# Kernel tuning notes

Hardware: AMD Instinct MI355X
Metric: run time of the kernel (lower is better)

The kernel has to match this reference:

```python
import jax, jax.numpy as jnp
import numpy as np

NUM_ROUTING_ITER = 3

def _squash(x):
    # Faithful to torch x.norm(): GLOBAL Frobenius norm over the whole tensor.
    n2 = jnp.sum(x * x)
    return x * (jnp.sqrt(n2) / (1.0 + n2))

def setup_inputs() -> dict:
    key = jax.random.key(0)
    k1, k2 = jax.random.split(key)
    x = jax.random.normal(k1, (256, 1152, 8), dtype=jnp.float32)
    weight = jax.random.normal(k2, (10, 1152, 8, 16), dtype=jnp.float32)
    return {"x": x, "weight": weight}

def reference(x, weight):
    # priors: [NC, B, IC, 1, OC] from [1,B,IC,1,L] @ [NC,1,IC,L,OC]
    priors = jnp.einsum('bil,nilo->nbio', x, weight)[:, :, :, None, :]
    b = jnp.zeros_like(priors)
    v = None
    for _ in range(NUM_ROUTING_ITER):
        # legacy F.softmax with no dim on a 5D tensor -> dim=1 (batch dim)
        c = jax.nn.softmax(b, axis=1)
        s = jnp.sum(c * priors, axis=2, keepdims=True)  # [NC,B,1,1,OC]
        v = _squash(s)
        b = b + jnp.sum(priors * v, axis=-1, keepdims=True)
    return v
```

## Files before the change

kernel.cpp:

```cpp
#include <hip/hip_runtime.h>
#include <math.h>

#define NC    10
#define BATCH 256
#define IC    1152
#define LDIM  8
#define OC    16

#define NCH   96
#define CH    (IC/NCH)
#define NBLK  (NC*NCH)
#define NTHR  256
#define NTOT  (NC*BATCH*OC)
#define NRED  160
#define KPG   (NCH/4)

typedef float f32x2 __attribute__((ext_vector_type(2)));

__device__ __forceinline__ int xcd_swizzle(int bid, int nwg) {
    int cpx = nwg >> 3;
    return (bid & 7) * cpx + (bid >> 3);
}

__global__ __launch_bounds__(256) void k0_xT(const float* __restrict__ x,
                                             float* __restrict__ xT)
{
    int u = blockIdx.x * 256 + threadIdx.x;
    int i = u >> 9, r = u & 511, b = r >> 1, h = r & 1;
    reinterpret_cast<float4*>(xT)[u] =
        reinterpret_cast<const float4*>(x)[((size_t)b * IC + i) * 2 + h];
}

__global__ __launch_bounds__(256) void kA(
    const float* __restrict__ xT, const float* __restrict__ w,
    float* __restrict__ s_part)
{
    int wg = xcd_swizzle(blockIdx.x, NBLK);
    int n  = wg / NCH, ch = wg % NCH;
    int i0 = ch * CH;
    int t  = threadIdx.x;

    f32x2 sp2[8];
#pragma unroll
    for (int j = 0; j < 8; ++j) sp2[j] = (f32x2){0.f, 0.f};

    for (int ii = 0; ii < CH; ++ii) {
        int i = i0 + ii;
        const float4* xp = reinterpret_cast<const float4*>(xT)
                         + ((size_t)i * BATCH + t) * 2;
        float4 xa = xp[0], xb = xp[1];
        float xr[8] = {xa.x, xa.y, xa.z, xa.w, xb.x, xb.y, xb.z, xb.w};
        const f32x2* wp2 = reinterpret_cast<const f32x2*>(
            w + (size_t)__builtin_amdgcn_readfirstlane((n * IC + i) * (LDIM * OC)));
#pragma unroll
        for (int l = 0; l < LDIM; ++l) {
            f32x2 xl = {xr[l], xr[l]};
#pragma unroll
            for (int j = 0; j < 8; ++j)
                sp2[j] += wp2[l * 8 + j] * xl;
        }
    }
    float4* dst = reinterpret_cast<float4*>(s_part)
                + (((size_t)ch * NC + n) * BATCH + t) * 4;
    const float inv = 1.0f / 256.0f;
    dst[0] = make_float4(sp2[0].x*inv, sp2[0].y*inv, sp2[1].x*inv, sp2[1].y*inv);
    dst[1] = make_float4(sp2[2].x*inv, sp2[2].y*inv, sp2[3].x*inv, sp2[3].y*inv);
    dst[2] = make_float4(sp2[4].x*inv, sp2[4].y*inv, sp2[5].x*inv, sp2[5].y*inv);
    dst[3] = make_float4(sp2[6].x*inv, sp2[6].y*inv, sp2[7].x*inv, sp2[7].y*inv);
}

__global__ __launch_bounds__(256) void kR(const float* __restrict__ s_part,
                                          float* __restrict__ s,
                                          float* __restrict__ n2_part)
{
    __shared__ float4 lds[4][64];
    int t = threadIdx.x, lane = t & 63, g = t >> 6;
    int idx0 = blockIdx.x * 256;
    const float* base = s_part + idx0 + lane * 4;
    float4 a0 = make_float4(0,0,0,0), a1 = a0, a2 = a0, a3 = a0;
    for (int k = 0; k < KPG; k += 4) {
        float4 v0 = *reinterpret_cast<const float4*>(base + (size_t)(g*KPG + k    ) * NTOT);
        float4 v1 = *reinterpret_cast<const float4*>(base + (size_t)(g*KPG + k + 1) * NTOT);
        float4 v2 = *reinterpret_cast<const float4*>(base + (size_t)(g*KPG + k + 2) * NTOT);
        float4 v3 = *reinterpret_cast<const float4*>(base + (size_t)(g*KPG + k + 3) * NTOT);
        a0.x += v0.x; a0.y += v0.y; a0.z += v0.z; a0.w += v0.w;
        a1.x += v1.x; a1.y += v1.y; a1.z += v1.z; a1.w += v1.w;
        a2.x += v2.x; a2.y += v2.y; a2.z += v2.z; a2.w += v2.w;
        a3.x += v3.x; a3.y += v3.y; a3.z += v3.z; a3.w += v3.w;
    }
    float4 a = make_float4((a0.x+a1.x)+(a2.x+a3.x), (a0.y+a1.y)+(a2.y+a3.y),
                           (a0.z+a1.z)+(a2.z+a3.z), (a0.w+a1.w)+(a2.w+a3.w));
    lds[g][lane] = a;
    __syncthreads();
    if (t < 64) {
        float4 s0 = lds[0][t], s1 = lds[1][t], s2 = lds[2][t], s3 = lds[3][t];
        float4 sv = make_float4((s0.x+s1.x)+(s2.x+s3.x), (s0.y+s1.y)+(s2.y+s3.y),
                                (s0.z+s1.z)+(s2.z+s3.z), (s0.w+s1.w)+(s2.w+s3.w));
        *reinterpret_cast<float4*>(s + idx0 + t * 4) = sv;
        float q = sv.x*sv.x + sv.y*sv.y + sv.z*sv.z + sv.w*sv.w;
#pragma unroll
        for (int m = 32; m >= 1; m >>= 1) q += __shfl_xor(q, m, 64);
        if (t == 0) n2_part[blockIdx.x] = q;
    }
}

template<int MODE>
__global__ __launch_bounds__(256) void kB(
    const float* __restrict__ xT, const float* __restrict__ w,
    const float* __restrict__ s1, const float* __restrict__ n2p1,
    const float* __restrict__ s2, const float* __restrict__ n2p2,
    float* __restrict__ s_part)
{
    __shared__ float e_lds[CH][NTHR];
    __shared__ float esW[CH][4];
    __shared__ float redW[8];
    int t = threadIdx.x, lane = t & 63, wid = t >> 6;
    int wg = xcd_swizzle(blockIdx.x, NBLK);
    int n  = wg / NCH, ch = wg % NCH;
    int i0 = ch * CH;

    float q1 = (t < NRED) ? n2p1[t] : 0.f;
    float q2 = (MODE == 2 && t < NRED) ? n2p2[t] : 0.f;
#pragma unroll
    for (int m = 32; m >= 1; m >>= 1) {
        q1 += __shfl_xor(q1, m, 64);
        if (MODE == 2) q2 += __shfl_xor(q2, m, 64);
    }
    if (lane == 0) { redW[wid] = q1; redW[4 + wid] = q2; }
    __syncthreads();
    float n2a = (redW[0] + redW[1]) + (redW[2] + redW[3]);
    float sc1 = sqrtf(n2a) / (1.0f + n2a);

    f32x2 v2[8];
    {
        const f32x2* s1p = reinterpret_cast<const f32x2*>(s1)
                         + ((size_t)n * BATCH + t) * 8;
        f32x2 sv = {sc1, sc1};
#pragma unroll
        for (int j = 0; j < 8; ++j) v2[j] = s1p[j] * sv;
        if (MODE == 2) {
            float n2b = (redW[4] + redW[5]) + (redW[6] + redW[7]);
            float sc2 = sqrtf(n2b) / (1.0f + n2b);
            const f32x2* s2p = reinterpret_cast<const f32x2*>(s2)
                             + ((size_t)n * BATCH + t) * 8;
            f32x2 sw = {sc2, sc2};
#pragma unroll
            for (int j = 0; j < 8; ++j) v2[j] += s2p[j] * sw;
        }
    }

    for (int ii = 0; ii < CH; ++ii) {
        int i = i0 + ii;
        const float4* xp = reinterpret_cast<const float4*>(xT)
                         + ((size_t)i * BATCH + t) * 2;
        float4 xa = xp[0], xb = xp[1];
        float xr[8] = {xa.x, xa.y, xa.z, xa.w, xb.x, xb.y, xb.z, xb.w};
        const f32x2* wp2 = reinterpret_cast<const f32x2*>(
            w + (size_t)__builtin_amdgcn_readfirstlane((n * IC + i) * (LDIM * OC)));
        f32x2 p2[8];
#pragma unroll
        for (int j = 0; j < 8; ++j) p2[j] = (f32x2){0.f, 0.f};
#pragma unroll
        for (int l = 0; l < LDIM; ++l) {
            f32x2 xl = {xr[l], xr[l]};
#pragma unroll
            for (int j = 0; j < 8; ++j)
                p2[j] += wp2[l * 8 + j] * xl;
        }
        f32x2 d2 = p2[0] * v2[0];
#pragma unroll
        for (int j = 1; j < 8; ++j) d2 += p2[j] * v2[j];
        float e = __expf(d2.x + d2.y);
        e_lds[ii][t] = e;
        float es = e;
#pragma unroll
        for (int m = 1; m < 64; m <<= 1) es += __shfl_xor(es, m, 64);
        if (lane == 0) esW[ii][wid] = es;
    }
    __syncthreads();

    f32x2 sp2[8];
#pragma unroll
    for (int j = 0; j < 8; ++j) sp2[j] = (f32x2){0.f, 0.f};

    for (int ii = 0; ii < CH; ++ii) {
        int i = i0 + ii;
        const float4* xp = reinterpret_cast<const float4*>(xT)
                         + ((size_t)i * BATCH + t) * 2;
        float4 xa = xp[0], xb = xp[1];
        float xr[8] = {xa.x, xa.y, xa.z, xa.w, xb.x, xb.y, xb.z, xb.w};
        const f32x2* wp2 = reinterpret_cast<const f32x2*>(
            w + (size_t)__builtin_amdgcn_readfirstlane((n * IC + i) * (LDIM * OC)));
        f32x2 p2[8];
#pragma unroll
        for (int j = 0; j < 8; ++j) p2[j] = (f32x2){0.f, 0.f};
#pragma unroll
        for (int l = 0; l < LDIM; ++l) {
            f32x2 xl = {xr[l], xr[l]};
#pragma unroll
            for (int j = 0; j < 8; ++j)
                p2[j] += wp2[l * 8 + j] * xl;
        }
        float denom = (esW[ii][0] + esW[ii][1]) + (esW[ii][2] + esW[ii][3]);
        float c = e_lds[ii][t] * (1.0f / denom);
        f32x2 c2 = {c, c};
#pragma unroll
        for (int j = 0; j < 8; ++j) sp2[j] += c2 * p2[j];
    }

    float4* dst = reinterpret_cast<float4*>(s_part)
                + (((size_t)ch * NC + n) * BATCH + t) * 4;
    dst[0] = make_float4(sp2[0].x, sp2[0].y, sp2[1].x, sp2[1].y);
    dst[1] = make_float4(sp2[2].x, sp2[2].y, sp2[3].x, sp2[3].y);
    dst[2] = make_float4(sp2[4].x, sp2[4].y, sp2[5].x, sp2[5].y);
    dst[3] = make_float4(sp2[6].x, sp2[6].y, sp2[7].x, sp2[7].y);
}

__global__ __launch_bounds__(256) void k_out(const float* __restrict__ s,
                                             const float* __restrict__ n2_part,
                                             float* __restrict__ out)
{
    __shared__ float redW[4];
    int t = threadIdx.x, lane = t & 63, wid = t >> 6;
    float q = (t < NRED) ? n2_part[t] : 0.f;
#pragma unroll
    for (int m = 32; m >= 1; m >>= 1) q += __shfl_xor(q, m, 64);
    if (lane == 0) redW[wid] = q;
    __syncthreads();
    float n2 = (redW[0] + redW[1]) + (redW[2] + redW[3]);
    float sc = sqrtf(n2) / (1.0f + n2);
    int idx = blockIdx.x * 256 + t;
    out[idx] = s[idx] * sc;
}

extern "C" void kernel_launch(void* const* d_in, const int* in_sizes, int n_in,
                              void* d_out, int out_size, void* d_ws, size_t ws_size,
                              hipStream_t stream)
{
    const float* x = (const float*)d_in[0];
    const float* w = (const float*)d_in[1];
    float* out = (float*)d_out;
    float* ws  = (float*)d_ws;

    float* xT      = ws;
    float* s_part  = xT + (size_t)IC * BATCH * LDIM;
    float* s1      = s_part + (size_t)NCH * NTOT;
    float* s2      = s1 + NTOT;
    float* s3      = s2 + NTOT;
    float* n2p1    = s3 + NTOT;
    float* n2p2    = n2p1 + NRED;
    float* n2p3    = n2p2 + NRED;

    dim3 blk(256);

    k0_xT<<<2304, blk, 0, stream>>>(x, xT);
    kA<<<NBLK, blk, 0, stream>>>(xT, w, s_part);
    kR<<<NRED, blk, 0, stream>>>(s_part, s1, n2p1);
    kB<1><<<NBLK, blk, 0, stream>>>(xT, w, s1, n2p1, s1, n2p1, s_part);
    kR<<<NRED, blk, 0, stream>>>(s_part, s2, n2p2);
    kB<2><<<NBLK, blk, 0, stream>>>(xT, w, s1, n2p1, s2, n2p2, s_part);
    kR<<<NRED, blk, 0, stream>>>(s_part, s3, n2p3);
    k_out<<<NRED, blk, 0, stream>>>(s3, n2p3, out);
}
```

Measured before the change: 114.5 us.

## Fuse softmax and weighted-sum passes, processing two input capsules per iteration

```diff
diff --git a/kernel.cpp b/kernel.cpp
--- a/kernel.cpp
+++ b/kernel.cpp
@@ -111,8 +111,7 @@
     const float* __restrict__ s2, const float* __restrict__ n2p2,
     float* __restrict__ s_part)
 {
-    __shared__ float e_lds[CH][NTHR];
-    __shared__ float esW[CH][4];
+    __shared__ float redA[2][2][4];
     __shared__ float redW[8];
     int t = threadIdx.x, lane = t & 63, wid = t >> 6;
     int wg = xcd_swizzle(blockIdx.x, NBLK);
@@ -149,63 +148,56 @@
         }
     }
 
-    for (int ii = 0; ii < CH; ++ii) {
-        int i = i0 + ii;
+    f32x2 sp2[8];
+#pragma unroll
+    for (int j = 0; j < 8; ++j) sp2[j] = (f32x2){0.f, 0.f};
+
+    for (int pr = 0; pr < CH / 2; ++pr) {
+        int i = i0 + 2 * pr;
         const float4* xp = reinterpret_cast<const float4*>(xT)
                          + ((size_t)i * BATCH + t) * 2;
-        float4 xa = xp[0], xb = xp[1];
-        float xr[8] = {xa.x, xa.y, xa.z, xa.w, xb.x, xb.y, xb.z, xb.w};
+        float4 xa0 = xp[0], xb0 = xp[1];
+        float4 xa1 = xp[2 * BATCH], xb1 = xp[2 * BATCH + 1];
+        float xr0[8] = {xa0.x, xa0.y, xa0.z, xa0.w, xb0.x, xb0.y, xb0.z, xb0.w};
+        float xr1[8] = {xa1.x, xa1.y, xa1.z, xa1.w, xb1.x, xb1.y, xb1.z, xb1.w};
         const f32x2* wp2 = reinterpret_cast<const f32x2*>(
             w + (size_t)__builtin_amdgcn_readfirstlane((n * IC + i) * (LDIM * OC)));
-        f32x2 p2[8];
-#pragma unroll
-        for (int j = 0; j < 8; ++j) p2[j] = (f32x2){0.f, 0.f};
+
+        f32x2 pA[8], pB[8];
+#pragma unroll
+        for (int j = 0; j < 8; ++j) { pA[j] = (f32x2){0.f,0.f}; pB[j] = (f32x2){0.f,0.f}; }
 #pragma unroll
         for (int l = 0; l < LDIM; ++l) {
-            f32x2 xl = {xr[l], xr[l]};
-#pragma unroll
-            for (int j = 0; j < 8; ++j)
-                p2[j] += wp2[l * 8 + j] * xl;
-        }
-        f32x2 d2 = p2[0] * v2[0];
-#pragma unroll
-        for (int j = 1; j < 8; ++j) d2 += p2[j] * v2[j];
-        float e = __expf(d2.x + d2.y);
-        e_lds[ii][t] = e;
-        float es = e;
-#pragma unroll
-        for (int m = 1; m < 64; m <<= 1) es += __shfl_xor(es, m, 64);
-        if (lane == 0) esW[ii][wid] = es;
-    }
-    __syncthreads();
-
-    f32x2 sp2[8];
-#pragma unroll
-    for (int j = 0; j < 8; ++j) sp2[j] = (f32x2){0.f, 0.f};
-
-    for (int ii = 0; ii < CH; ++ii) {
-        int i = i0 + ii;
-        const float4* xp = reinterpret_cast<const float4*>(xT)
-                         + ((size_t)i * BATCH + t) * 2;
-        float4 xa = xp[0], xb = xp[1];
-        float xr[8] = {xa.x, xa.y, xa.z, xa.w, xb.x, xb.y, xb.z, xb.w};
-        const f32x2* wp2 = reinterpret_cast<const f32x2*>(
-            w + (size_t)__builtin_amdgcn_readfirstlane((n * IC + i) * (LDIM * OC)));
-        f32x2 p2[8];
-#pragma unroll
-        for (int j = 0; j < 8; ++j) p2[j] = (f32x2){0.f, 0.f};
-#pragma unroll
-        for (int l = 0; l < LDIM; ++l) {
-            f32x2 xl = {xr[l], xr[l]};
-#pragma unroll
-            for (int j = 0; j < 8; ++j)
-                p2[j] += wp2[l * 8 + j] * xl;
-        }
-        float denom = (esW[ii][0] + esW[ii][1]) + (esW[ii][2] + esW[ii][3]);
-        float c = e_lds[ii][t] * (1.0f / denom);
-        f32x2 c2 = {c, c};
-#pragma unroll
-        for (int j = 0; j < 8; ++j) sp2[j] += c2 * p2[j];
+            f32x2 x0 = {xr0[l], xr0[l]}, x1 = {xr1[l], xr1[l]};
+#pragma unroll
+            for (int j = 0; j < 8; ++j) {
+                pA[j] += wp2[l * 8 + j] * x0;
+                pB[j] += wp2[64 + l * 8 + j] * x1;
+            }
+        }
+
+        f32x2 dA = pA[0] * v2[0], dB = pB[0] * v2[0];
+#pragma unroll
+        for (int j = 1; j < 8; ++j) { dA += pA[j] * v2[j]; dB += pB[j] * v2[j]; }
+        float betaA = dA.x + dA.y, betaB = dB.x + dB.y;
+
+        float eA = __expf(betaA), eB = __expf(betaB);
+        float esA = eA, esB = eB;
+#pragma unroll
+        for (int m = 1; m < 64; m <<= 1) {
+            esA += __shfl_xor(esA, m, 64);
+            esB += __shfl_xor(esB, m, 64);
+        }
+        if (lane == 0) { redA[pr & 1][0][wid] = esA; redA[pr & 1][1][wid] = esB; }
+        __syncthreads();
+        float denA = (redA[pr&1][0][0] + redA[pr&1][0][1])
+                   + (redA[pr&1][0][2] + redA[pr&1][0][3]);
+        float denB = (redA[pr&1][1][0] + redA[pr&1][1][1])
+                   + (redA[pr&1][1][2] + redA[pr&1][1][3]);
+        float cA = eA / denA, cB = eB / denB;
+        f32x2 cA2 = {cA, cA}, cB2 = {cB, cB};
+#pragma unroll
+        for (int j = 0; j < 8; ++j) sp2[j] += cA2 * pA[j] + cB2 * pB[j];
     }
 
     float4* dst = reinterpret_cast<float4*>(s_part)
```

Result: faster. 94.28 us, median of 2 (-17.7%).
